# Kernel optimization log

Measured on AMD Instinct MI355X. Metric: run time of the kernel, lower is better.

## Reference

```python
import jax, jax.numpy as jnp
import numpy as np

B, SRC = 32, 1024
SEQ_LEN, CONTEXT_LEN, D_MODEL, VOCAB = 128, 5, 512, 32000


def setup_inputs() -> dict:
    key = jax.random.key(0)
    k1, k2, k3, k4, k5, k6 = jax.random.split(key, 6)
    x = jax.random.randint(k1, (B, SRC), 0, VOCAB, dtype=jnp.int64 if jax.config.jax_enable_x64 else jnp.int32)
    yc = jax.random.randint(k2, (B, SEQ_LEN * CONTEXT_LEN), 0, VOCAB, dtype=x.dtype)
    F_emb = jax.random.normal(k3, (VOCAB, D_MODEL), dtype=jnp.float32) * 0.02
    G_emb = jax.random.normal(k4, (VOCAB, D_MODEL), dtype=jnp.float32) * 0.02
    fan_in = CONTEXT_LEN * D_MODEL
    P_w = jax.random.uniform(k5, (fan_in, D_MODEL), dtype=jnp.float32,
                             minval=-1.0, maxval=1.0) * (fan_in ** -0.5)
    P_b = jnp.zeros((D_MODEL,), dtype=jnp.float32)
    return {"x": x, "yc": yc, "F_emb": F_emb, "G_emb": G_emb, "P_w": P_w, "P_b": P_b}


def reference(x, yc, F_emb, G_emb, P_w, P_b):
    # padding mask from source tokens: 1.0 where token == 0
    mask = (x == 0).astype(jnp.float32)                      # [B, SRC]
    xe = F_emb[x]                                            # [B, SRC, D]
    yce = G_emb[yc].reshape(-1, SEQ_LEN, CONTEXT_LEN * D_MODEL)  # [B, SEQ, C*D]
    py = jnp.einsum('bsk,kd->bsd', yce, P_w) + P_b           # Dense P(y): [B, SEQ, D]
    a = jnp.einsum('bxd,bsd->bxs', xe, py)                   # [B, SRC, SEQ]
    a = a + mask[:, :, None] * -1e9                          # mask padded source rows
    a = jnp.transpose(a, (0, 2, 1))                          # [B, SEQ, SRC]
    a = jax.nn.softmax(a, axis=-1)
    out = jnp.einsum('bsx,bxd->bsd', a, xe)                  # [B, SEQ, D]
    return (out, a)
```

## Files before the change

### kernel.cpp

```cpp
#include <hip/hip_runtime.h>
#include <hip/hip_bf16.h>
#include <stdint.h>

#define BATCH 32
#define SRCN 1024
#define SEQL 128
#define CTXN 5
#define DMOD 512

typedef __attribute__((ext_vector_type(8))) short short8;
typedef __attribute__((ext_vector_type(4))) float floatx4;

typedef __attribute__((address_space(3))) void lds_t;
typedef __attribute__((address_space(1))) void glb_t;

__device__ __forceinline__ void gload_lds16(const void* g, void* l) {
    __builtin_amdgcn_global_load_lds((const glb_t*)g, (lds_t*)l, 16, 0, 0);
}

__device__ __forceinline__ ushort f2b(float f) {
    __hip_bfloat16 h = __float2bfloat16(f);
    return *reinterpret_cast<ushort*>(&h);
}

#define LSLOT(m, sg) ((((m) << 3) | ((sg) ^ ((m) & 7))) << 3)

__global__ __launch_bounds__(256) void k_yce(
    const int* __restrict__ yc, const float* __restrict__ G,
    ushort* __restrict__ yce)
{
    const int r = blockIdx.x;
    const int b = r >> 7, s = r & 127;
    const int tid = threadIdx.x;
    for (int i = tid; i < 640; i += 256) {
        const int c = i >> 7;
        const int tok = yc[b * (SEQL * CTXN) + s * CTXN + c];
        const float4 v = *(const float4*)(G + (size_t)tok * DMOD + (i & 127) * 4);
        ushort4 o;
        o.x = f2b(v.x); o.y = f2b(v.y); o.z = f2b(v.z); o.w = f2b(v.w);
        *(ushort4*)(yce + (size_t)r * 2560 + i * 4) = o;
    }
}

__global__ __launch_bounds__(256) void k_pwt(
    const float* __restrict__ Pw, ushort* __restrict__ Pwt)
{
    __shared__ float t[64][68];
    const int k0 = blockIdx.x * 64, n0 = blockIdx.y * 64;
    const int tid = threadIdx.x;
    #pragma unroll
    for (int it = 0; it < 4; ++it) {
        const int c = tid + it * 256;
        const int kr = c >> 4, c4 = c & 15;
        const float4 v = *(const float4*)(Pw + (size_t)(k0 + kr) * DMOD + n0 + c4 * 4);
        t[kr][c4 * 4 + 0] = v.x; t[kr][c4 * 4 + 1] = v.y;
        t[kr][c4 * 4 + 2] = v.z; t[kr][c4 * 4 + 3] = v.w;
    }
    __syncthreads();
    #pragma unroll
    for (int it = 0; it < 2; ++it) {
        const int c = tid + it * 256;
        const int n = c >> 3, seg = c & 7;
        ushort4 o0, o1;
        o0.x = f2b(t[seg * 8 + 0][n]); o0.y = f2b(t[seg * 8 + 1][n]);
        o0.z = f2b(t[seg * 8 + 2][n]); o0.w = f2b(t[seg * 8 + 3][n]);
        o1.x = f2b(t[seg * 8 + 4][n]); o1.y = f2b(t[seg * 8 + 5][n]);
        o1.z = f2b(t[seg * 8 + 6][n]); o1.w = f2b(t[seg * 8 + 7][n]);
        ushort* dst = Pwt + (size_t)(n0 + n) * 2560 + k0 + seg * 8;
        *(ushort4*)dst = o0; *(ushort4*)(dst + 4) = o1;
    }
}

__global__ __launch_bounds__(256) void k_gemm_py(
    const ushort* __restrict__ yce, const ushort* __restrict__ pwt,
    float* __restrict__ part)
{
    __shared__ ushort As[8 * 512];
    __shared__ ushort Bs[8 * 512];
    const int f = blockIdx.x;
    const int n  = (f >> 3) & 7;
    const int m  = (f & 7) | (((f >> 6) & 7) << 3);
    const int ks = f >> 9;
    const int tid = threadIdx.x;
    const int w = tid >> 6, lane = tid & 63;
    const int l15 = lane & 15, q = lane >> 4;
    const int wm = w >> 1, wn = w & 1;
    const int m0 = m * 64, n0 = n * 64, koff = ks * 1280;

    const int sr = lane >> 3;
    const int ssg = ((lane & 7) ^ sr) * 8;

    const ushort* Abase = yce + (size_t)(m0 + sr) * 2560 + koff + ssg;
    const ushort* Bbase = pwt + (size_t)(n0 + sr) * 2560 + koff + ssg;

    floatx4 acc[2][2];
    #pragma unroll
    for (int mi = 0; mi < 2; ++mi)
        #pragma unroll
        for (int ni = 0; ni < 2; ++ni)
            acc[mi][ni] = (floatx4){0.f, 0.f, 0.f, 0.f};

    for (int kk = 0; kk < 1280; kk += 64) {
        __syncthreads();
        #pragma unroll
        for (int i = 0; i < 2; ++i) {
            const int cc = w * 2 + i;
            gload_lds16(Abase + (size_t)(cc * 8) * 2560 + kk, (void*)(As + cc * 512));
            gload_lds16(Bbase + (size_t)(cc * 8) * 2560 + kk, (void*)(Bs + cc * 512));
        }
        __syncthreads();
        #pragma unroll
        for (int s2 = 0; s2 < 2; ++s2) {
            const int sg = s2 * 4 + q;
            short8 af[2], bf[2];
            #pragma unroll
            for (int mi = 0; mi < 2; ++mi)
                af[mi] = *(const short8*)(As + LSLOT(wm * 32 + mi * 16 + l15, sg));
            #pragma unroll
            for (int ni = 0; ni < 2; ++ni)
                bf[ni] = *(const short8*)(Bs + LSLOT(wn * 32 + ni * 16 + l15, sg));
            #pragma unroll
            for (int mi = 0; mi < 2; ++mi)
                #pragma unroll
                for (int ni = 0; ni < 2; ++ni)
                    acc[mi][ni] = __builtin_amdgcn_mfma_f32_16x16x32_bf16(
                        af[mi], bf[ni], acc[mi][ni], 0, 0, 0);
        }
    }

    float* dst = part + (size_t)ks * (4096LL * DMOD);
    #pragma unroll
    for (int ni = 0; ni < 2; ++ni) {
        const int col = n0 + wn * 32 + ni * 16 + l15;
        #pragma unroll
        for (int mi = 0; mi < 2; ++mi) {
            const int row0 = m0 + wm * 32 + mi * 16 + q * 4;
            #pragma unroll
            for (int r = 0; r < 4; ++r)
                dst[(size_t)(row0 + r) * DMOD + col] = acc[mi][ni][r];
        }
    }
}

__global__ __launch_bounds__(256) void k_red2(
    const float* __restrict__ part, const float* __restrict__ Pb,
    ushort* __restrict__ py)
{
    const long long SL = 4096LL * DMOD;
    const int i = blockIdx.x * 256 + threadIdx.x;
    const float4 a = *(const float4*)(part + (size_t)i * 4);
    const float4 b = *(const float4*)(part + SL + (size_t)i * 4);
    const float4 bias = *(const float4*)(Pb + ((i * 4) & 511));
    ushort4 o;
    o.x = f2b(a.x + b.x + bias.x);
    o.y = f2b(a.y + b.y + bias.y);
    o.z = f2b(a.z + b.z + bias.z);
    o.w = f2b(a.w + b.w + bias.w);
    *(ushort4*)(py + (size_t)i * 4) = o;
}

__global__ __launch_bounds__(256) void k_xe2(
    const int* __restrict__ x, const float* __restrict__ F,
    ushort* __restrict__ xe, ushort* __restrict__ xet)
{
    __shared__ ushort t[64][72];
    const int z = blockIdx.z;
    const int x0 = blockIdx.x * 64, d0 = blockIdx.y * 64;
    const int tid = threadIdx.x;
    #pragma unroll
    for (int it = 0; it < 4; ++it) {
        const int c = tid + it * 256;
        const int row = c >> 4, seg = c & 15;
        const int tok = x[z * SRCN + x0 + row];
        const float4 v = *(const float4*)(F + (size_t)tok * DMOD + d0 + seg * 4);
        ushort4 o;
        o.x = f2b(v.x); o.y = f2b(v.y); o.z = f2b(v.z); o.w = f2b(v.w);
        *(ushort4*)&t[row][seg * 4] = o;
        *(ushort4*)(xe + (size_t)(z * SRCN + x0 + row) * DMOD + d0 + seg * 4) = o;
    }
    __syncthreads();
    #pragma unroll
    for (int it = 0; it < 2; ++it) {
        const int c = tid + it * 256;
        const int d = c >> 3, seg = c & 7;
        ushort4 o0, o1;
        o0.x = t[seg * 8 + 0][d]; o0.y = t[seg * 8 + 1][d];
        o0.z = t[seg * 8 + 2][d]; o0.w = t[seg * 8 + 3][d];
        o1.x = t[seg * 8 + 4][d]; o1.y = t[seg * 8 + 5][d];
        o1.z = t[seg * 8 + 6][d]; o1.w = t[seg * 8 + 7][d];
        ushort* dst = xet + (size_t)(z * DMOD + d0 + d) * SRCN + x0 + seg * 8;
        *(ushort4*)dst = o0; *(ushort4*)(dst + 4) = o1;
    }
}

__global__ __launch_bounds__(256) void k_gemm_sc(
    const ushort* __restrict__ py, const int* __restrict__ x,
    const ushort* __restrict__ xe, float* __restrict__ a_out)
{
    __shared__ ushort As[8 * 512];
    __shared__ ushort Bs[4 * 512];
    const int f = blockIdx.x;
    const int h = f >> 3;
    const int n = h & 31;
    const int m = (h >> 5) & 1;
    const int b = (f & 7) + 8 * (h >> 6);
    const int tid = threadIdx.x;
    const int w = tid >> 6, lane = tid & 63;
    const int l15 = lane & 15, q = lane >> 4;
    const int wm = w >> 1, wn = w & 1;
    const int m0 = m * 64, n0 = n * 32;

    const int sr = lane >> 3;
    const int ssg = ((lane & 7) ^ sr) * 8;

    const ushort* Abase = py + (size_t)(b * SEQL + m0 + sr) * DMOD + ssg;
    const ushort* Bbase = xe + (size_t)(b * SRCN + n0 + sr) * DMOD + ssg;

    floatx4 acc[2];
    acc[0] = (floatx4){0.f, 0.f, 0.f, 0.f};
    acc[1] = (floatx4){0.f, 0.f, 0.f, 0.f};

    for (int kk = 0; kk < DMOD; kk += 64) {
        __syncthreads();
        #pragma unroll
        for (int i = 0; i < 2; ++i) {
            const int cc = w * 2 + i;
            gload_lds16(Abase + (size_t)(cc * 8) * DMOD + kk, (void*)(As + cc * 512));
        }
        gload_lds16(Bbase + (size_t)(w * 8) * DMOD + kk, (void*)(Bs + w * 512));
        __syncthreads();
        #pragma unroll
        for (int s2 = 0; s2 < 2; ++s2) {
            const int sg = s2 * 4 + q;
            short8 af[2], bf;
            af[0] = *(const short8*)(As + LSLOT(wm * 32 + l15, sg));
            af[1] = *(const short8*)(As + LSLOT(wm * 32 + 16 + l15, sg));
            bf    = *(const short8*)(Bs + LSLOT(wn * 16 + l15, sg));
            acc[0] = __builtin_amdgcn_mfma_f32_16x16x32_bf16(af[0], bf, acc[0], 0, 0, 0);
            acc[1] = __builtin_amdgcn_mfma_f32_16x16x32_bf16(af[1], bf, acc[1], 0, 0, 0);
        }
    }

    const int col = n0 + wn * 16 + l15;
    const float msk = (x[b * SRCN + col] == 0) ? -1e9f : 0.0f;
    #pragma unroll
    for (int mi = 0; mi < 2; ++mi) {
        const int row0 = m0 + wm * 32 + mi * 16 + q * 4;
        #pragma unroll
        for (int r = 0; r < 4; ++r)
            a_out[((size_t)b * SEQL + row0 + r) * SRCN + col] = acc[mi][r] + msk;
    }
}

__global__ __launch_bounds__(256) void k_softmax(
    float* __restrict__ a, ushort* __restrict__ abf)
{
    const int row = blockIdx.x;
    float* p = a + (size_t)row * SRCN;
    ushort* pb = abf + (size_t)row * SRCN;
    const int tid = threadIdx.x;
    const int wave = tid >> 6, lane = tid & 63;

    float4 v = *(const float4*)(p + tid * 4);

    float mx = fmaxf(fmaxf(v.x, v.y), fmaxf(v.z, v.w));
    #pragma unroll
    for (int off = 32; off > 0; off >>= 1)
        mx = fmaxf(mx, __shfl_down(mx, off, 64));
    __shared__ float redm[4];
    if (lane == 0) redm[wave] = mx;
    __syncthreads();
    mx = fmaxf(fmaxf(redm[0], redm[1]), fmaxf(redm[2], redm[3]));

    const float e0 = __expf(v.x - mx);
    const float e1 = __expf(v.y - mx);
    const float e2 = __expf(v.z - mx);
    const float e3 = __expf(v.w - mx);

    float sm = e0 + e1 + e2 + e3;
    #pragma unroll
    for (int off = 32; off > 0; off >>= 1)
        sm += __shfl_down(sm, off, 64);
    __shared__ float reds[4];
    if (lane == 0) reds[wave] = sm;
    __syncthreads();
    sm = reds[0] + reds[1] + reds[2] + reds[3];

    const float inv = 1.0f / sm;
    float4 o;
    o.x = e0 * inv; o.y = e1 * inv; o.z = e2 * inv; o.w = e3 * inv;
    *(float4*)(p + tid * 4) = o;
    ushort4 ob;
    ob.x = f2b(o.x); ob.y = f2b(o.y); ob.z = f2b(o.z); ob.w = f2b(o.w);
    *(ushort4*)(pb + tid * 4) = ob;
}

__global__ __launch_bounds__(256) void k_gemm_out(
    const ushort* __restrict__ abf, const ushort* __restrict__ xet,
    float* __restrict__ outp)
{
    __shared__ ushort As[4 * 512];
    __shared__ ushort Bs[8 * 512];
    const int f = blockIdx.x;
    const int h = f >> 3;
    const int n = h & 7;
    const int m = (h >> 3) & 3;
    const int b = (f & 7) + 8 * (h >> 5);
    const int tid = threadIdx.x;
    const int w = tid >> 6, lane = tid & 63;
    const int l15 = lane & 15, q = lane >> 4;
    const int wm = w >> 1, wn = w & 1;
    const int m0 = m * 32, n0 = n * 64;

    const int sr = lane >> 3;
    const int ssg = ((lane & 7) ^ sr) * 8;

    const ushort* Abase = abf + (size_t)(b * SEQL + m0 + sr) * SRCN + ssg;
    const ushort* Bbase = xet + (size_t)(b * DMOD + n0 + sr) * SRCN + ssg;

    floatx4 acc[2];
    acc[0] = (floatx4){0.f, 0.f, 0.f, 0.f};
    acc[1] = (floatx4){0.f, 0.f, 0.f, 0.f};

    for (int kk = 0; kk < SRCN; kk += 64) {
        __syncthreads();
        gload_lds16(Abase + (size_t)(w * 8) * SRCN + kk, (void*)(As + w * 512));
        #pragma unroll
        for (int i = 0; i < 2; ++i) {
            const int cc = w * 2 + i;
            gload_lds16(Bbase + (size_t)(cc * 8) * SRCN + kk, (void*)(Bs + cc * 512));
        }
        __syncthreads();
        #pragma unroll
        for (int s2 = 0; s2 < 2; ++s2) {
            const int sg = s2 * 4 + q;
            short8 af, bf[2];
            af    = *(const short8*)(As + LSLOT(wm * 16 + l15, sg));
            bf[0] = *(const short8*)(Bs + LSLOT(wn * 32 + l15, sg));
            bf[1] = *(const short8*)(Bs + LSLOT(wn * 32 + 16 + l15, sg));
            acc[0] = __builtin_amdgcn_mfma_f32_16x16x32_bf16(af, bf[0], acc[0], 0, 0, 0);
            acc[1] = __builtin_amdgcn_mfma_f32_16x16x32_bf16(af, bf[1], acc[1], 0, 0, 0);
        }
    }

    const int row0 = m0 + wm * 16 + q * 4;
    #pragma unroll
    for (int ni = 0; ni < 2; ++ni) {
        const int col = n0 + wn * 32 + ni * 16 + l15;
        #pragma unroll
        for (int r = 0; r < 4; ++r)
            outp[((size_t)b * SEQL + row0 + r) * DMOD + col] = acc[ni][r];
    }
}

extern "C" void kernel_launch(void* const* d_in, const int* in_sizes, int n_in,
                              void* d_out, int out_size, void* d_ws, size_t ws_size,
                              hipStream_t stream)
{
    const int*   x    = (const int*)d_in[0];
    const int*   yc   = (const int*)d_in[1];
    const float* Femb = (const float*)d_in[2];
    const float* Gemb = (const float*)d_in[3];
    const float* Pw   = (const float*)d_in[4];
    const float* Pb   = (const float*)d_in[5];

    float* out_p = (float*)d_out;
    float* a_p   = out_p + (size_t)BATCH * SEQL * DMOD;

    char* ws = (char*)d_ws;
    ushort* yce  = (ushort*)(ws);
    ushort* pwt  = (ushort*)(ws + 20971520);
    float*  part = (float*) (ws + 23592960);
    ushort* xe   = (ushort*)(ws);
    ushort* xet  = (ushort*)(ws + 33554432);
    ushort* py   = (ushort*)(ws + 67108864);
    ushort* abf  = (ushort*)(ws + 71303168);

    dim3 blk(256);
    k_yce<<<dim3(4096), blk, 0, stream>>>(yc, Gemb, yce);
    k_pwt<<<dim3(40, 8), blk, 0, stream>>>(Pw, pwt);

    k_gemm_py<<<dim3(1024), blk, 0, stream>>>(yce, pwt, part);
    k_red2<<<dim3(2048), blk, 0, stream>>>(part, Pb, py);

    k_xe2<<<dim3(16, 8, 32), blk, 0, stream>>>(x, Femb, xe, xet);

    k_gemm_sc<<<dim3(2048), blk, 0, stream>>>(py, x, xe, a_p);
    k_softmax<<<dim3(4096), blk, 0, stream>>>(a_p, abf);
    k_gemm_out<<<dim3(1024), blk, 0, stream>>>(abf, xet, out_p);
}
```

Before: 223.7 us.

## Merge prep kernels, enlarge GEMM tiles, use 4-way split-K for projection

Fuses the yce gather and Pw transpose into one launch. The projection GEMM moves to 128x64 tiles with 4-way split-K and a 4-partial reduction. The score GEMM now uses 128x64 tiles and the output GEMM 64x64 tiles with 128-deep K steps. Larger tiles raise MFMA work per LDS load and cut redundant global traffic and launch overhead, at the cost of fewer blocks, more registers and a larger split-K partial buffer.

```diff
diff --git a/kernel.cpp b/kernel.cpp
--- a/kernel.cpp
+++ b/kernel.cpp
@@ -25,49 +25,48 @@
 
 #define LSLOT(m, sg) ((((m) << 3) | ((sg) ^ ((m) & 7))) << 3)
 
-__global__ __launch_bounds__(256) void k_yce(
+__global__ __launch_bounds__(256) void k_prep(
     const int* __restrict__ yc, const float* __restrict__ G,
-    ushort* __restrict__ yce)
-{
-    const int r = blockIdx.x;
-    const int b = r >> 7, s = r & 127;
-    const int tid = threadIdx.x;
-    for (int i = tid; i < 640; i += 256) {
-        const int c = i >> 7;
-        const int tok = yc[b * (SEQL * CTXN) + s * CTXN + c];
-        const float4 v = *(const float4*)(G + (size_t)tok * DMOD + (i & 127) * 4);
-        ushort4 o;
-        o.x = f2b(v.x); o.y = f2b(v.y); o.z = f2b(v.z); o.w = f2b(v.w);
-        *(ushort4*)(yce + (size_t)r * 2560 + i * 4) = o;
-    }
-}
-
-__global__ __launch_bounds__(256) void k_pwt(
+    ushort* __restrict__ yce,
     const float* __restrict__ Pw, ushort* __restrict__ Pwt)
 {
-    __shared__ float t[64][68];
-    const int k0 = blockIdx.x * 64, n0 = blockIdx.y * 64;
-    const int tid = threadIdx.x;
-    #pragma unroll
-    for (int it = 0; it < 4; ++it) {
-        const int c = tid + it * 256;
-        const int kr = c >> 4, c4 = c & 15;
-        const float4 v = *(const float4*)(Pw + (size_t)(k0 + kr) * DMOD + n0 + c4 * 4);
-        t[kr][c4 * 4 + 0] = v.x; t[kr][c4 * 4 + 1] = v.y;
-        t[kr][c4 * 4 + 2] = v.z; t[kr][c4 * 4 + 3] = v.w;
-    }
-    __syncthreads();
-    #pragma unroll
-    for (int it = 0; it < 2; ++it) {
-        const int c = tid + it * 256;
-        const int n = c >> 3, seg = c & 7;
-        ushort4 o0, o1;
-        o0.x = f2b(t[seg * 8 + 0][n]); o0.y = f2b(t[seg * 8 + 1][n]);
-        o0.z = f2b(t[seg * 8 + 2][n]); o0.w = f2b(t[seg * 8 + 3][n]);
-        o1.x = f2b(t[seg * 8 + 4][n]); o1.y = f2b(t[seg * 8 + 5][n]);
-        o1.z = f2b(t[seg * 8 + 6][n]); o1.w = f2b(t[seg * 8 + 7][n]);
-        ushort* dst = Pwt + (size_t)(n0 + n) * 2560 + k0 + seg * 8;
-        *(ushort4*)dst = o0; *(ushort4*)(dst + 4) = o1;
+    const int tid = threadIdx.x;
+    if (blockIdx.x < 4096) {
+        const int r = blockIdx.x;
+        const int b = r >> 7, s = r & 127;
+        for (int i = tid; i < 640; i += 256) {
+            const int c = i >> 7;
+            const int tok = yc[b * (SEQL * CTXN) + s * CTXN + c];
+            const float4 v = *(const float4*)(G + (size_t)tok * DMOD + (i & 127) * 4);
+            ushort4 o;
+            o.x = f2b(v.x); o.y = f2b(v.y); o.z = f2b(v.z); o.w = f2b(v.w);
+            *(ushort4*)(yce + (size_t)r * 2560 + i * 4) = o;
+        }
+    } else {
+        __shared__ float t[64][68];
+        const int bid = blockIdx.x - 4096;
+        const int k0 = (bid % 40) * 64, n0 = (bid / 40) * 64;
+        #pragma unroll
+        for (int it = 0; it < 4; ++it) {
+            const int c = tid + it * 256;
+            const int kr = c >> 4, c4 = c & 15;
+            const float4 v = *(const float4*)(Pw + (size_t)(k0 + kr) * DMOD + n0 + c4 * 4);
+            t[kr][c4 * 4 + 0] = v.x; t[kr][c4 * 4 + 1] = v.y;
+            t[kr][c4 * 4 + 2] = v.z; t[kr][c4 * 4 + 3] = v.w;
+        }
+        __syncthreads();
+        #pragma unroll
+        for (int it = 0; it < 2; ++it) {
+            const int c = tid + it * 256;
+            const int n = c >> 3, seg = c & 7;
+            ushort4 o0, o1;
+            o0.x = f2b(t[seg * 8 + 0][n]); o0.y = f2b(t[seg * 8 + 1][n]);
+            o0.z = f2b(t[seg * 8 + 2][n]); o0.w = f2b(t[seg * 8 + 3][n]);
+            o1.x = f2b(t[seg * 8 + 4][n]); o1.y = f2b(t[seg * 8 + 5][n]);
+            o1.z = f2b(t[seg * 8 + 6][n]); o1.w = f2b(t[seg * 8 + 7][n]);
+            ushort* dst = Pwt + (size_t)(n0 + n) * 2560 + k0 + seg * 8;
+            *(ushort4*)dst = o0; *(ushort4*)(dst + 4) = o1;
+        }
     }
 }
 
@@ -75,17 +74,19 @@
     const ushort* __restrict__ yce, const ushort* __restrict__ pwt,
     float* __restrict__ part)
 {
-    __shared__ ushort As[8 * 512];
+    __shared__ ushort As[16 * 512];
     __shared__ ushort Bs[8 * 512];
     const int f = blockIdx.x;
-    const int n  = (f >> 3) & 7;
-    const int m  = (f & 7) | (((f >> 6) & 7) << 3);
-    const int ks = f >> 9;
+    const int mlo = f & 7;
+    const int n   = (f >> 3) & 7;
+    const int mhi = (f >> 6) & 3;
+    const int ks  = f >> 8;
+    const int m = mlo | (mhi << 3);
     const int tid = threadIdx.x;
     const int w = tid >> 6, lane = tid & 63;
     const int l15 = lane & 15, q = lane >> 4;
     const int wm = w >> 1, wn = w & 1;
-    const int m0 = m * 64, n0 = n * 64, koff = ks * 1280;
+    const int m0 = m * 128, n0 = n * 64, koff = ks * 640;
 
     const int sr = lane >> 3;
     const int ssg = ((lane & 7) ^ sr) * 8;
@@ -93,34 +94,38 @@
     const ushort* Abase = yce + (size_t)(m0 + sr) * 2560 + koff + ssg;
     const ushort* Bbase = pwt + (size_t)(n0 + sr) * 2560 + koff + ssg;
 
-    floatx4 acc[2][2];
-    #pragma unroll
-    for (int mi = 0; mi < 2; ++mi)
+    floatx4 acc[4][2];
+    #pragma unroll
+    for (int mi = 0; mi < 4; ++mi)
         #pragma unroll
         for (int ni = 0; ni < 2; ++ni)
             acc[mi][ni] = (floatx4){0.f, 0.f, 0.f, 0.f};
 
-    for (int kk = 0; kk < 1280; kk += 64) {
-        __syncthreads();
+    for (int kk = 0; kk < 640; kk += 64) {
+        __syncthreads();
+        #pragma unroll
+        for (int i = 0; i < 4; ++i) {
+            const int cc = w * 4 + i;
+            gload_lds16(Abase + (size_t)(cc * 8) * 2560 + kk, (void*)(As + cc * 512));
+        }
         #pragma unroll
         for (int i = 0; i < 2; ++i) {
             const int cc = w * 2 + i;
-            gload_lds16(Abase + (size_t)(cc * 8) * 2560 + kk, (void*)(As + cc * 512));
             gload_lds16(Bbase + (size_t)(cc * 8) * 2560 + kk, (void*)(Bs + cc * 512));
         }
         __syncthreads();
         #pragma unroll
         for (int s2 = 0; s2 < 2; ++s2) {
             const int sg = s2 * 4 + q;
-            short8 af[2], bf[2];
-            #pragma unroll
-            for (int mi = 0; mi < 2; ++mi)
-                af[mi] = *(const short8*)(As + LSLOT(wm * 32 + mi * 16 + l15, sg));
+            short8 af[4], bf[2];
+            #pragma unroll
+            for (int mi = 0; mi < 4; ++mi)
+                af[mi] = *(const short8*)(As + LSLOT(wm * 64 + mi * 16 + l15, sg));
             #pragma unroll
             for (int ni = 0; ni < 2; ++ni)
                 bf[ni] = *(const short8*)(Bs + LSLOT(wn * 32 + ni * 16 + l15, sg));
             #pragma unroll
-            for (int mi = 0; mi < 2; ++mi)
+            for (int mi = 0; mi < 4; ++mi)
                 #pragma unroll
                 for (int ni = 0; ni < 2; ++ni)
                     acc[mi][ni] = __builtin_amdgcn_mfma_f32_16x16x32_bf16(
@@ -133,8 +138,8 @@
     for (int ni = 0; ni < 2; ++ni) {
         const int col = n0 + wn * 32 + ni * 16 + l15;
         #pragma unroll
-        for (int mi = 0; mi < 2; ++mi) {
-            const int row0 = m0 + wm * 32 + mi * 16 + q * 4;
+        for (int mi = 0; mi < 4; ++mi) {
+            const int row0 = m0 + wm * 64 + mi * 16 + q * 4;
             #pragma unroll
             for (int r = 0; r < 4; ++r)
                 dst[(size_t)(row0 + r) * DMOD + col] = acc[mi][ni][r];
@@ -142,7 +147,7 @@
     }
 }
 
-__global__ __launch_bounds__(256) void k_red2(
+__global__ __launch_bounds__(256) void k_red4(
     const float* __restrict__ part, const float* __restrict__ Pb,
     ushort* __restrict__ py)
 {
@@ -150,12 +155,14 @@
     const int i = blockIdx.x * 256 + threadIdx.x;
     const float4 a = *(const float4*)(part + (size_t)i * 4);
     const float4 b = *(const float4*)(part + SL + (size_t)i * 4);
+    const float4 c = *(const float4*)(part + 2 * SL + (size_t)i * 4);
+    const float4 d = *(const float4*)(part + 3 * SL + (size_t)i * 4);
     const float4 bias = *(const float4*)(Pb + ((i * 4) & 511));
     ushort4 o;
-    o.x = f2b(a.x + b.x + bias.x);
-    o.y = f2b(a.y + b.y + bias.y);
-    o.z = f2b(a.z + b.z + bias.z);
-    o.w = f2b(a.w + b.w + bias.w);
+    o.x = f2b(a.x + b.x + c.x + d.x + bias.x);
+    o.y = f2b(a.y + b.y + c.y + d.y + bias.y);
+    o.z = f2b(a.z + b.z + c.z + d.z + bias.z);
+    o.w = f2b(a.w + b.w + c.w + d.w + bias.w);
     *(ushort4*)(py + (size_t)i * 4) = o;
 }
 
@@ -197,58 +204,74 @@
     const ushort* __restrict__ py, const int* __restrict__ x,
     const ushort* __restrict__ xe, float* __restrict__ a_out)
 {
-    __shared__ ushort As[8 * 512];
-    __shared__ ushort Bs[4 * 512];
+    __shared__ ushort As[16 * 512];
+    __shared__ ushort Bs[8 * 512];
     const int f = blockIdx.x;
-    const int h = f >> 3;
-    const int n = h & 31;
-    const int m = (h >> 5) & 1;
-    const int b = (f & 7) + 8 * (h >> 6);
+    const int g = f >> 3;
+    const int b = ((g & 3) << 3) | (f & 7);
+    const int n = g >> 2;
     const int tid = threadIdx.x;
     const int w = tid >> 6, lane = tid & 63;
     const int l15 = lane & 15, q = lane >> 4;
     const int wm = w >> 1, wn = w & 1;
-    const int m0 = m * 64, n0 = n * 32;
+    const int n0 = n * 64;
 
     const int sr = lane >> 3;
     const int ssg = ((lane & 7) ^ sr) * 8;
 
-    const ushort* Abase = py + (size_t)(b * SEQL + m0 + sr) * DMOD + ssg;
+    const ushort* Abase = py + (size_t)(b * SEQL + sr) * DMOD + ssg;
     const ushort* Bbase = xe + (size_t)(b * SRCN + n0 + sr) * DMOD + ssg;
 
-    floatx4 acc[2];
-    acc[0] = (floatx4){0.f, 0.f, 0.f, 0.f};
-    acc[1] = (floatx4){0.f, 0.f, 0.f, 0.f};
+    floatx4 acc[4][2];
+    #pragma unroll
+    for (int mi = 0; mi < 4; ++mi)
+        #pragma unroll
+        for (int ni = 0; ni < 2; ++ni)
+            acc[mi][ni] = (floatx4){0.f, 0.f, 0.f, 0.f};
 
     for (int kk = 0; kk < DMOD; kk += 64) {
         __syncthreads();
+        #pragma unroll
+        for (int i = 0; i < 4; ++i) {
+            const int cc = w * 4 + i;
+            gload_lds16(Abase + (size_t)(cc * 8) * DMOD + kk, (void*)(As + cc * 512));
+        }
         #pragma unroll
         for (int i = 0; i < 2; ++i) {
             const int cc = w * 2 + i;
-            gload_lds16(Abase + (size_t)(cc * 8) * DMOD + kk, (void*)(As + cc * 512));
-        }
-        gload_lds16(Bbase + (size_t)(w * 8) * DMOD + kk, (void*)(Bs + w * 512));
+            gload_lds16(Bbase + (size_t)(cc * 8) * DMOD + kk, (void*)(Bs + cc * 512));
+        }
         __syncthreads();
         #pragma unroll
         for (int s2 = 0; s2 < 2; ++s2) {
             const int sg = s2 * 4 + q;
-            short8 af[2], bf;
-            af[0] = *(const short8*)(As + LSLOT(wm * 32 + l15, sg));
-            af[1] = *(const short8*)(As + LSLOT(wm * 32 + 16 + l15, sg));
-            bf    = *(const short8*)(Bs + LSLOT(wn * 16 + l15, sg));
-            acc[0] = __builtin_amdgcn_mfma_f32_16x16x32_bf16(af[0], bf, acc[0], 0, 0, 0);
-            acc[1] = __builtin_amdgcn_mfma_f32_16x16x32_bf16(af[1], bf, acc[1], 0, 0, 0);
-        }
-    }
-
-    const int col = n0 + wn * 16 + l15;
-    const float msk = (x[b * SRCN + col] == 0) ? -1e9f : 0.0f;
-    #pragma unroll
-    for (int mi = 0; mi < 2; ++mi) {
-        const int row0 = m0 + wm * 32 + mi * 16 + q * 4;
-        #pragma unroll
-        for (int r = 0; r < 4; ++r)
-            a_out[((size_t)b * SEQL + row0 + r) * SRCN + col] = acc[mi][r] + msk;
+            short8 af[4], bf[2];
+            #pragma unroll
+            for (int mi = 0; mi < 4; ++mi)
+                af[mi] = *(const short8*)(As + LSLOT(wm * 64 + mi * 16 + l15, sg));
+            #pragma unroll
+            for (int ni = 0; ni < 2; ++ni)
+                bf[ni] = *(const short8*)(Bs + LSLOT(wn * 32 + ni * 16 + l15, sg));
+            #pragma unroll
+            for (int mi = 0; mi < 4; ++mi)
+                #pragma unroll
+                for (int ni = 0; ni < 2; ++ni)
+                    acc[mi][ni] = __builtin_amdgcn_mfma_f32_16x16x32_bf16(
+                        af[mi], bf[ni], acc[mi][ni], 0, 0, 0);
+        }
+    }
+
+    #pragma unroll
+    for (int ni = 0; ni < 2; ++ni) {
+        const int col = n0 + wn * 32 + ni * 16 + l15;
+        const float msk = (x[b * SRCN + col] == 0) ? -1e9f : 0.0f;
+        #pragma unroll
+        for (int mi = 0; mi < 4; ++mi) {
+            const int row0 = wm * 64 + mi * 16 + q * 4;
+            #pragma unroll
+            for (int r = 0; r < 4; ++r)
+                a_out[((size_t)b * SEQL + row0 + r) * SRCN + col] = acc[mi][ni][r] + msk;
+        }
     }
 }
 
@@ -299,18 +322,18 @@
     const ushort* __restrict__ abf, const ushort* __restrict__ xet,
     float* __restrict__ outp)
 {
-    __shared__ ushort As[4 * 512];
-    __shared__ ushort Bs[8 * 512];
+    __shared__ ushort As[2 * 8 * 512];
+    __shared__ ushort Bs[2 * 8 * 512];
     const int f = blockIdx.x;
-    const int h = f >> 3;
-    const int n = h & 7;
-    const int m = (h >> 3) & 3;
-    const int b = (f & 7) + 8 * (h >> 5);
+    const int g = f >> 3;
+    const int b = ((g & 3) << 3) | (f & 7);
+    const int h = g >> 2;
+    const int m = h & 1, n = h >> 1;
     const int tid = threadIdx.x;
     const int w = tid >> 6, lane = tid & 63;
     const int l15 = lane & 15, q = lane >> 4;
     const int wm = w >> 1, wn = w & 1;
-    const int m0 = m * 32, n0 = n * 64;
+    const int m0 = m * 64, n0 = n * 64;
 
     const int sr = lane >> 3;
     const int ssg = ((lane & 7) ^ sr) * 8;
@@ -318,38 +341,59 @@
     const ushort* Abase = abf + (size_t)(b * SEQL + m0 + sr) * SRCN + ssg;
     const ushort* Bbase = xet + (size_t)(b * DMOD + n0 + sr) * SRCN + ssg;
 
-    floatx4 acc[2];
-    acc[0] = (floatx4){0.f, 0.f, 0.f, 0.f};
-    acc[1] = (floatx4){0.f, 0.f, 0.f, 0.f};
-
-    for (int kk = 0; kk < SRCN; kk += 64) {
-        __syncthreads();
-        gload_lds16(Abase + (size_t)(w * 8) * SRCN + kk, (void*)(As + w * 512));
-        #pragma unroll
-        for (int i = 0; i < 2; ++i) {
-            const int cc = w * 2 + i;
-            gload_lds16(Bbase + (size_t)(cc * 8) * SRCN + kk, (void*)(Bs + cc * 512));
-        }
-        __syncthreads();
-        #pragma unroll
-        for (int s2 = 0; s2 < 2; ++s2) {
-            const int sg = s2 * 4 + q;
-            short8 af, bf[2];
-            af    = *(const short8*)(As + LSLOT(wm * 16 + l15, sg));
-            bf[0] = *(const short8*)(Bs + LSLOT(wn * 32 + l15, sg));
-            bf[1] = *(const short8*)(Bs + LSLOT(wn * 32 + 16 + l15, sg));
-            acc[0] = __builtin_amdgcn_mfma_f32_16x16x32_bf16(af, bf[0], acc[0], 0, 0, 0);
-            acc[1] = __builtin_amdgcn_mfma_f32_16x16x32_bf16(af, bf[1], acc[1], 0, 0, 0);
-        }
-    }
-
-    const int row0 = m0 + wm * 16 + q * 4;
+    floatx4 acc[2][2];
+    #pragma unroll
+    for (int mi = 0; mi < 2; ++mi)
+        #pragma unroll
+        for (int ni = 0; ni < 2; ++ni)
+            acc[mi][ni] = (floatx4){0.f, 0.f, 0.f, 0.f};
+
+    for (int kk = 0; kk < SRCN; kk += 128) {
+        __syncthreads();
+        #pragma unroll
+        for (int sub = 0; sub < 2; ++sub) {
+            #pragma unroll
+            for (int i = 0; i < 2; ++i) {
+                const int cc = w * 2 + i;
+                gload_lds16(Abase + (size_t)(cc * 8) * SRCN + kk + sub * 64,
+                            (void*)(As + sub * 4096 + cc * 512));
+                gload_lds16(Bbase + (size_t)(cc * 8) * SRCN + kk + sub * 64,
+                            (void*)(Bs + sub * 4096 + cc * 512));
+            }
+        }
+        __syncthreads();
+        #pragma unroll
+        for (int sub = 0; sub < 2; ++sub) {
+            #pragma unroll
+            for (int s2 = 0; s2 < 2; ++s2) {
+                const int sg = s2 * 4 + q;
+                short8 af[2], bf[2];
+                #pragma unroll
+                for (int mi = 0; mi < 2; ++mi)
+                    af[mi] = *(const short8*)(As + sub * 4096 + LSLOT(wm * 32 + mi * 16 + l15, sg));
+                #pragma unroll
+                for (int ni = 0; ni < 2; ++ni)
+                    bf[ni] = *(const short8*)(Bs + sub * 4096 + LSLOT(wn * 32 + ni * 16 + l15, sg));
+                #pragma unroll
+                for (int mi = 0; mi < 2; ++mi)
+                    #pragma unroll
+                    for (int ni = 0; ni < 2; ++ni)
+                        acc[mi][ni] = __builtin_amdgcn_mfma_f32_16x16x32_bf16(
+                            af[mi], bf[ni], acc[mi][ni], 0, 0, 0);
+            }
+        }
+    }
+
     #pragma unroll
     for (int ni = 0; ni < 2; ++ni) {
         const int col = n0 + wn * 32 + ni * 16 + l15;
         #pragma unroll
-        for (int r = 0; r < 4; ++r)
-            outp[((size_t)b * SEQL + row0 + r) * DMOD + col] = acc[ni][r];
+        for (int mi = 0; mi < 2; ++mi) {
+            const int row0 = m0 + wm * 32 + mi * 16 + q * 4;
+            #pragma unroll
+            for (int r = 0; r < 4; ++r)
+                outp[((size_t)b * SEQL + row0 + r) * DMOD + col] = acc[mi][ni][r];
+        }
     }
 }
 
@@ -377,15 +421,14 @@
     ushort* abf  = (ushort*)(ws + 71303168);
 
     dim3 blk(256);
-    k_yce<<<dim3(4096), blk, 0, stream>>>(yc, Gemb, yce);
-    k_pwt<<<dim3(40, 8), blk, 0, stream>>>(Pw, pwt);
+    k_prep<<<dim3(4416), blk, 0, stream>>>(yc, Gemb, yce, Pw, pwt);
 
     k_gemm_py<<<dim3(1024), blk, 0, stream>>>(yce, pwt, part);
-    k_red2<<<dim3(2048), blk, 0, stream>>>(part, Pb, py);
+    k_red4<<<dim3(2048), blk, 0, stream>>>(part, Pb, py);
 
     k_xe2<<<dim3(16, 8, 32), blk, 0, stream>>>(x, Femb, xe, xet);
 
-    k_gemm_sc<<<dim3(2048), blk, 0, stream>>>(py, x, xe, a_p);
+    k_gemm_sc<<<dim3(512), blk, 0, stream>>>(py, x, xe, a_p);
     k_softmax<<<dim3(4096), blk, 0, stream>>>(a_p, abf);
-    k_gemm_out<<<dim3(1024), blk, 0, stream>>>(abf, xet, out_p);
-}
+    k_gemm_out<<<dim3(512), blk, 0, stream>>>(abf, xet, out_p);
+}
```

New measurement: 220.5 us. No clear change (-1.4%).
